# Performance work log

Measured on AMD Instinct MI355X. Metric: run time of the kernel, lower is better.

Reference implementation:

```python
import jax, jax.numpy as jnp
import numpy as np

OFFSET = 1e-6   # undefined global in source; small positive stabilizer
COS_EPS = 1e-8  # F.cosine_similarity default eps

B, N, M = 128, 2048, 128


def setup_inputs() -> dict:
    key = jax.random.key(0)
    ks = jax.random.split(key, 9)
    return {
        "memory": jax.random.normal(ks[0], (B, N, M), jnp.float32),
        "k_t": jax.random.normal(ks[1], (B, M), jnp.float32),
        "beta_t": jax.random.uniform(ks[2], (B,), jnp.float32),
        "g_t": jax.random.uniform(ks[3], (B,), jnp.float32),
        "w_t_minus_1": jax.random.uniform(ks[4], (B, N), jnp.float32),
        "s_t": jax.random.uniform(ks[5], (B, 3), jnp.float32),
        "gamma_t": jax.random.uniform(ks[6], (B,), jnp.float32),
        "e_t": jax.random.uniform(ks[7], (B, M), jnp.float32),
        "a_t": jax.random.normal(ks[8], (B, M), jnp.float32),
    }


def reference(memory, k_t, beta_t, g_t, w_t_minus_1, s_t, gamma_t, e_t, a_t):
    # ---- content_addressing (faithful to source, incl. w_tilde_t = w_{t-1} quirk) ----
    mk = memory + OFFSET                     # [B,N,M]
    kk = k_t[:, None, :] + OFFSET            # [B,1,M]
    dot = jnp.sum(mk * kk, axis=-1)          # [B,N]
    nm = jnp.maximum(jnp.sqrt(jnp.sum(mk * mk, -1)), COS_EPS)            # [B,N]
    nk = jnp.maximum(jnp.sqrt(jnp.sum(kk * kk, -1)), COS_EPS)            # [B,1]
    K = dot / (nm * nk)                      # cosine similarity, [B,N]
    w_c = jax.nn.softmax(beta_t[:, None] * K, axis=1)                    # [B,N]
    w_g = g_t[:, None] * w_c + (1.0 - g_t[:, None]) * w_t_minus_1        # [B,N]
    w_pow = w_t_minus_1 ** gamma_t[:, None]                              # sharpening on w_{t-1}
    w_t = jnp.sum(w_pow, axis=1, keepdims=True) + OFFSET                 # [B,1]
    w_t = jnp.broadcast_to(w_t, w_t_minus_1.shape)                       # [B,N] (source .repeat)

    # ---- writing: rank-1 erase/add memory update ----
    erase = w_t[:, :, None] * e_t[:, None, :]                            # [B,N,M]
    M_new = memory * (1.0 - erase) + w_t[:, :, None] * a_t[:, None, :]   # [B,N,M]

    # ---- reading ----
    r_t = jnp.einsum('bn,bnm->bm', w_t, M_new)                           # [B,M]

    # single concatenated output so every chain stays live: [B, M + 2N]
    return jnp.concatenate([r_t, w_t, w_g], axis=1)
```

## Files before the change

### kernel.cpp

```cpp
#include <hip/hip_runtime.h>
#include <hip/hip_bf16.h>
#include <math.h>

#define BB 128
#define NN 2048
#define MM 128
#define ROWS_PER_BLOCK 128
#define OFFSET_EPS 1e-6f
#define COS_EPS 1e-8f

__global__ __launch_bounds__(256) void pass_a(
    const float* __restrict__ memory, const float* __restrict__ k_t,
    const float* __restrict__ beta_t, float* __restrict__ colsum,
    float* __restrict__ score)
{
    const int blocks_per_b = NN / ROWS_PER_BLOCK;
    const int b     = blockIdx.x / blocks_per_b;
    const int r0    = (blockIdx.x % blocks_per_b) * ROWS_PER_BLOCK;
    const int wave  = threadIdx.x >> 6;
    const int lane  = threadIdx.x & 63;

    float2 kraw = *(const float2*)(k_t + b * MM + 2 * lane);
    const float kx = kraw.x + OFFSET_EPS;
    const float ky = kraw.y + OFFSET_EPS;

    float nks = kx * kx + ky * ky;
    #pragma unroll
    for (int s = 32; s; s >>= 1) nks += __shfl_xor(nks, s);
    const float nk = fmaxf(sqrtf(nks), COS_EPS);
    const float beta_over_nk = beta_t[b] / nk;

    const float* mbase = memory + (size_t)b * NN * MM;
    float cs_x = 0.f, cs_y = 0.f;

    #pragma unroll 4
    for (int i = 0; i < ROWS_PER_BLOCK / 4; ++i) {
        const int n = r0 + wave + 4 * i;
        float2 mv = *(const float2*)(mbase + (size_t)n * MM + 2 * lane);
        cs_x += mv.x;
        cs_y += mv.y;
        const float vx = mv.x + OFFSET_EPS;
        const float vy = mv.y + OFFSET_EPS;
        float dot = vx * kx + vy * ky;
        float sq  = vx * vx + vy * vy;
        #pragma unroll
        for (int s = 32; s; s >>= 1) {
            dot += __shfl_xor(dot, s);
            sq  += __shfl_xor(sq,  s);
        }
        if (lane == 0) {
            const float nm = fmaxf(sqrtf(sq), COS_EPS);
            score[b * NN + n] = dot * beta_over_nk / nm;
        }
    }

    __shared__ float s_col[4][MM];
    s_col[wave][2 * lane]     = cs_x;
    s_col[wave][2 * lane + 1] = cs_y;
    __syncthreads();
    if (threadIdx.x < MM) {
        const float v = s_col[0][threadIdx.x] + s_col[1][threadIdx.x] +
                        s_col[2][threadIdx.x] + s_col[3][threadIdx.x];
        atomicAdd(colsum + b * MM + threadIdx.x, v);
    }
}

__global__ __launch_bounds__(256) void pass_b(
    const float* __restrict__ score,  const float* __restrict__ g_t,
    const float* __restrict__ w_prev, const float* __restrict__ gamma_t,
    const float* __restrict__ e_t,    const float* __restrict__ a_t,
    const float* __restrict__ colsum, float* __restrict__ out)
{
    const int b   = blockIdx.x;
    const int tid = threadIdx.x;
    __shared__ float red[256];

    float sc[8];
    float mx = -INFINITY;
    #pragma unroll
    for (int i = 0; i < 8; ++i) {
        sc[i] = score[b * NN + tid + 256 * i];
        mx = fmaxf(mx, sc[i]);
    }
    red[tid] = mx; __syncthreads();
    for (int s = 128; s; s >>= 1) {
        if (tid < s) red[tid] = fmaxf(red[tid], red[tid + s]);
        __syncthreads();
    }
    mx = red[0]; __syncthreads();

    float sum = 0.f;
    #pragma unroll
    for (int i = 0; i < 8; ++i) {
        sc[i] = expf(sc[i] - mx);
        sum += sc[i];
    }
    red[tid] = sum; __syncthreads();
    for (int s = 128; s; s >>= 1) {
        if (tid < s) red[tid] += red[tid + s];
        __syncthreads();
    }
    const float inv_sum = 1.f / red[0];
    __syncthreads();

    const float g     = g_t[b];
    const float gamma = gamma_t[b];
    float wg[8];
    float psum = 0.f;
    #pragma unroll
    for (int i = 0; i < 8; ++i) {
        const float w = w_prev[b * NN + tid + 256 * i];
        wg[i] = g * (sc[i] * inv_sum) + (1.f - g) * w;
        psum += powf(w, gamma);
    }
    red[tid] = psum; __syncthreads();
    for (int s = 128; s; s >>= 1) {
        if (tid < s) red[tid] += red[tid + s];
        __syncthreads();
    }
    const float S = red[0] + OFFSET_EPS;

    float* orow = out + (size_t)b * (MM + 2 * NN);
    #pragma unroll
    for (int i = 0; i < 8; ++i) {
        const int n = tid + 256 * i;
        orow[MM + n]      = S;
        orow[MM + NN + n] = wg[i];
    }
    if (tid < MM) {
        const float cs = colsum[b * MM + tid];
        const float r  = S * ((1.f - S * e_t[b * MM + tid]) * cs +
                              (float)NN * S * a_t[b * MM + tid]);
        orow[tid] = r;
    }
}

extern "C" void kernel_launch(void* const* d_in, const int* in_sizes, int n_in,
                              void* d_out, int out_size, void* d_ws, size_t ws_size,
                              hipStream_t stream) {
    const float* memory  = (const float*)d_in[0];
    const float* k_t     = (const float*)d_in[1];
    const float* beta_t  = (const float*)d_in[2];
    const float* g_t     = (const float*)d_in[3];
    const float* w_prev  = (const float*)d_in[4];
    const float* gamma_t = (const float*)d_in[6];
    const float* e_t     = (const float*)d_in[7];
    const float* a_t     = (const float*)d_in[8];
    float* out = (float*)d_out;

    float* colsum = (float*)d_ws;
    float* score  = colsum + BB * MM;

    hipMemsetAsync(colsum, 0, BB * MM * sizeof(float), stream);

    const int grid_a = BB * (NN / ROWS_PER_BLOCK);
    pass_a<<<grid_a, 256, 0, stream>>>(memory, k_t, beta_t, colsum, score);
    pass_b<<<BB, 256, 0, stream>>>(score, g_t, w_prev, gamma_t, e_t, a_t,
                                   colsum, out);
}
```

Measured before the change: 219.7 us.

## Use float4 row loads, per-chunk column partials, and fast exp/pow

Each lane now loads four floats so a half-wave covers one memory row, shortening the shuffle reduction and widening loads. Column sums are written to per-chunk partial buffers and summed in the second kernel, replacing atomics and removing the memset launch. The softmax exp and the sharpening pow use fast intrinsics, trading a little accuracy for cheaper math.

```diff
diff --git a/kernel.cpp b/kernel.cpp
--- a/kernel.cpp
+++ b/kernel.cpp
@@ -6,62 +6,68 @@
 #define NN 2048
 #define MM 128
 #define ROWS_PER_BLOCK 128
+#define CHUNKS (NN / ROWS_PER_BLOCK)
 #define OFFSET_EPS 1e-6f
 #define COS_EPS 1e-8f
 
 __global__ __launch_bounds__(256) void pass_a(
     const float* __restrict__ memory, const float* __restrict__ k_t,
-    const float* __restrict__ beta_t, float* __restrict__ colsum,
+    const float* __restrict__ beta_t, float* __restrict__ colsum_part,
     float* __restrict__ score)
 {
-    const int blocks_per_b = NN / ROWS_PER_BLOCK;
-    const int b     = blockIdx.x / blocks_per_b;
-    const int r0    = (blockIdx.x % blocks_per_b) * ROWS_PER_BLOCK;
+    const int b     = blockIdx.x / CHUNKS;
+    const int chunk = blockIdx.x % CHUNKS;
+    const int r0    = chunk * ROWS_PER_BLOCK;
     const int wave  = threadIdx.x >> 6;
     const int lane  = threadIdx.x & 63;
+    const int half  = lane >> 5;
+    const int l32   = lane & 31;
 
-    float2 kraw = *(const float2*)(k_t + b * MM + 2 * lane);
-    const float kx = kraw.x + OFFSET_EPS;
-    const float ky = kraw.y + OFFSET_EPS;
+    float4 kv = *(const float4*)(k_t + b * MM + 4 * l32);
+    const float k0 = kv.x + OFFSET_EPS, k1 = kv.y + OFFSET_EPS,
+                k2 = kv.z + OFFSET_EPS, k3 = kv.w + OFFSET_EPS;
 
-    float nks = kx * kx + ky * ky;
+    float nks = k0 * k0 + k1 * k1 + k2 * k2 + k3 * k3;
     #pragma unroll
-    for (int s = 32; s; s >>= 1) nks += __shfl_xor(nks, s);
+    for (int s = 16; s; s >>= 1) nks += __shfl_xor(nks, s);
     const float nk = fmaxf(sqrtf(nks), COS_EPS);
     const float beta_over_nk = beta_t[b] / nk;
 
     const float* mbase = memory + (size_t)b * NN * MM;
-    float cs_x = 0.f, cs_y = 0.f;
+    float cs0 = 0.f, cs1 = 0.f, cs2 = 0.f, cs3 = 0.f;
 
     #pragma unroll 4
-    for (int i = 0; i < ROWS_PER_BLOCK / 4; ++i) {
-        const int n = r0 + wave + 4 * i;
-        float2 mv = *(const float2*)(mbase + (size_t)n * MM + 2 * lane);
-        cs_x += mv.x;
-        cs_y += mv.y;
-        const float vx = mv.x + OFFSET_EPS;
-        const float vy = mv.y + OFFSET_EPS;
-        float dot = vx * kx + vy * ky;
-        float sq  = vx * vx + vy * vy;
+    for (int i = 0; i < ROWS_PER_BLOCK / 8; ++i) {
+        const int n = r0 + 8 * i + 2 * wave + half;
+        float4 mv = *(const float4*)(mbase + (size_t)n * MM + 4 * l32);
+        cs0 += mv.x; cs1 += mv.y; cs2 += mv.z; cs3 += mv.w;
+        const float v0 = mv.x + OFFSET_EPS, v1 = mv.y + OFFSET_EPS,
+                    v2 = mv.z + OFFSET_EPS, v3 = mv.w + OFFSET_EPS;
+        float dot = v0 * k0 + v1 * k1 + v2 * k2 + v3 * k3;
+        float sq  = v0 * v0 + v1 * v1 + v2 * v2 + v3 * v3;
         #pragma unroll
-        for (int s = 32; s; s >>= 1) {
+        for (int s = 16; s; s >>= 1) {
             dot += __shfl_xor(dot, s);
             sq  += __shfl_xor(sq,  s);
         }
-        if (lane == 0) {
+        if (l32 == 0) {
             const float nm = fmaxf(sqrtf(sq), COS_EPS);
             score[b * NN + n] = dot * beta_over_nk / nm;
         }
     }
 
-    __shared__ float s_col[4][MM];
-    s_col[wave][2 * lane]     = cs_x;
-    s_col[wave][2 * lane + 1] = cs_y;
+    __shared__ float s_col[8][MM];
+    const int hw = wave * 2 + half;
+    s_col[hw][4 * l32 + 0] = cs0;
+    s_col[hw][4 * l32 + 1] = cs1;
+    s_col[hw][4 * l32 + 2] = cs2;
+    s_col[hw][4 * l32 + 3] = cs3;
     __syncthreads();
     if (threadIdx.x < MM) {
-        const float v = s_col[0][threadIdx.x] + s_col[1][threadIdx.x] +
-                        s_col[2][threadIdx.x] + s_col[3][threadIdx.x];
-        atomicAdd(colsum + b * MM + threadIdx.x, v);
+        float v = 0.f;
+        #pragma unroll
+        for (int j = 0; j < 8; ++j) v += s_col[j][threadIdx.x];
+        colsum_part[(size_t)chunk * BB * MM + b * MM + threadIdx.x] = v;
     }
 }
 
@@ -69,7 +75,7 @@
     const float* __restrict__ score,  const float* __restrict__ g_t,
     const float* __restrict__ w_prev, const float* __restrict__ gamma_t,
     const float* __restrict__ e_t,    const float* __restrict__ a_t,
-    const float* __restrict__ colsum, float* __restrict__ out)
+    const float* __restrict__ colsum_part, float* __restrict__ out)
 {
     const int b   = blockIdx.x;
     const int tid = threadIdx.x;
@@ -92,7 +98,7 @@
     float sum = 0.f;
     #pragma unroll
     for (int i = 0; i < 8; ++i) {
-        sc[i] = expf(sc[i] - mx);
+        sc[i] = __expf(sc[i] - mx);
         sum += sc[i];
     }
     red[tid] = sum; __syncthreads();
@@ -111,7 +117,7 @@
     for (int i = 0; i < 8; ++i) {
         const float w = w_prev[b * NN + tid + 256 * i];
         wg[i] = g * (sc[i] * inv_sum) + (1.f - g) * w;
-        psum += powf(w, gamma);
+        psum += __powf(w, gamma);
     }
     red[tid] = psum; __syncthreads();
     for (int s = 128; s; s >>= 1) {
@@ -128,9 +134,12 @@
         orow[MM + NN + n] = wg[i];
     }
     if (tid < MM) {
-        const float cs = colsum[b * MM + tid];
-        const float r  = S * ((1.f - S * e_t[b * MM + tid]) * cs +
-                              (float)NN * S * a_t[b * MM + tid]);
+        float cs = 0.f;
+        #pragma unroll
+        for (int c = 0; c < CHUNKS; ++c)
+            cs += colsum_part[(size_t)c * BB * MM + b * MM + tid];
+        const float r = S * ((1.f - S * e_t[b * MM + tid]) * cs +
+                             (float)NN * S * a_t[b * MM + tid]);
         orow[tid] = r;
     }
 }
@@ -148,13 +157,11 @@
     const float* a_t     = (const float*)d_in[8];
     float* out = (float*)d_out;
 
-    float* colsum = (float*)d_ws;
-    float* score  = colsum + BB * MM;
+    float* colsum_part = (float*)d_ws;
+    float* score       = colsum_part + CHUNKS * BB * MM;
 
-    hipMemsetAsync(colsum, 0, BB * MM * sizeof(float), stream);
-
-    const int grid_a = BB * (NN / ROWS_PER_BLOCK);
-    pass_a<<<grid_a, 256, 0, stream>>>(memory, k_t, beta_t, colsum, score);
+    const int grid_a = BB * CHUNKS;
+    pass_a<<<grid_a, 256, 0, stream>>>(memory, k_t, beta_t, colsum_part, score);
     pass_b<<<BB, 256, 0, stream>>>(score, g_t, w_prev, gamma_t, e_t, a_t,
-                                   colsum, out);
+                                   colsum_part, out);
 }
```

New measurement: 214.7 us. 1.02x faster.
